# Kernel optimization log

Hardware: AMD Instinct MI355X
Metric: run time of the kernel (lower is better)

Reference implementation:

```python
import jax, jax.numpy as jnp
import numpy as np

V = 50000   # words_num
D = 128     # embedding_dim
B = 2048    # batch
P = 20      # max Huffman path length


def setup_inputs() -> dict:
    key = jax.random.key(0)
    k1, k2, k3, k4, k5 = jax.random.split(key, 5)
    inputs_vector = jax.random.uniform(k1, (B, V), dtype=jnp.float32)
    path_nodes_indices = jax.random.randint(k2, (B, P), 0, V)
    huffman_codes = jax.random.randint(k3, (B, P), 0, 2).astype(jnp.float32)
    mask = jnp.ones((B, P), dtype=jnp.float32)
    # learned params, torch nn.Linear weight layout [out, in], kaiming-uniform-ish scale
    W_emb = jax.random.uniform(k4, (D, V), dtype=jnp.float32, minval=-1.0, maxval=1.0) / np.sqrt(V)
    W_cls = jax.random.uniform(k5, (V, D), dtype=jnp.float32, minval=-1.0, maxval=1.0) / np.sqrt(D)
    return {
        "inputs_vector": inputs_vector,
        "W_emb": W_emb,
        "W_cls": W_cls,
        "path_nodes_indices": path_nodes_indices,
        "huffman_codes": huffman_codes,
        "mask": mask,
    }


def _bce_with_logits(logits, targets):
    # numerically stable, elementwise (reduction='none')
    return jnp.maximum(logits, 0.0) - logits * targets + jnp.log1p(jnp.exp(-jnp.abs(logits)))


def reference(inputs_vector, W_emb, W_cls, path_nodes_indices, huffman_codes, mask):
    x = inputs_vector @ W_emb.T              # [B, D]  embedding Linear (no bias)
    logits_full = x @ W_cls.T                # [B, V]  full-vocab cls matmul (as in source)
    logits = jnp.take_along_axis(logits_full, path_nodes_indices, axis=1)  # [B, P]
    loss = _bce_with_logits(logits, huffman_codes)  # [B, P]
    masked_loss = loss * mask
    per_sample = masked_loss.sum(axis=-1) / mask.sum(axis=-1)  # [B]
    return per_sample.mean()
```

## Files before the change

### kernel.cpp

```cpp
#include <hip/hip_runtime.h>
#include <hip/hip_bf16.h>

#define V 50000
#define D 128
#define B 2048
#define P 20

#define BM 256
#define BK 64
#define NSPLIT 64
#define KC 784
#define NMT (B / BM)

typedef float  f32x4   __attribute__((ext_vector_type(4)));
typedef short  bf16x8  __attribute__((ext_vector_type(8)));
typedef unsigned int uint4v __attribute__((ext_vector_type(4)));

__device__ __forceinline__ unsigned int pk2(float a, float b) {
    return (__float_as_uint(b) & 0xFFFF0000u) | (__float_as_uint(a) >> 16);
}
__device__ __forceinline__ unsigned short f2bf(float f) {
    unsigned int u = __float_as_uint(f);
    return (unsigned short)((u + 0x7FFFu + ((u >> 16) & 1u)) >> 16);
}
__device__ __forceinline__ bf16x8 pack8(f32x4 lo, f32x4 hi) {
    union { uint4v u; bf16x8 h; } r;
    r.u.x = pk2(lo[0], lo[1]); r.u.y = pk2(lo[2], lo[3]);
    r.u.z = pk2(hi[0], hi[1]); r.u.w = pk2(hi[2], hi[3]);
    return r.h;
}

__global__ __launch_bounds__(256)
void w2v_wcast(const float* __restrict__ Wemb, unsigned* __restrict__ Wb) {
    const size_t t = (size_t)blockIdx.x * 256 + threadIdx.x;
    const size_t base = t * 8;
    if (base >= (size_t)D * V) return;
    const f32x4* src = reinterpret_cast<const f32x4*>(Wemb + base);
    f32x4 v0 = src[0], v1 = src[1];
    uint4v u;
    u.x = pk2(v0[0], v0[1]); u.y = pk2(v0[2], v0[3]);
    u.z = pk2(v1[0], v1[1]); u.w = pk2(v1[2], v1[3]);
    *reinterpret_cast<uint4v*>(Wb + base / 2) = u;
}

template<int WBF>
__global__ __launch_bounds__(512, 4)
void w2v_gemm(const float* __restrict__ Ain, const void* __restrict__ Wsrc,
              void* __restrict__ part, int use_atomic) {
    __shared__ uint4v smem4[4096];
    char* smem = (char*)smem4;

    const int i   = blockIdx.x;
    const int xcd = i & 7;
    const int j   = i >> 3;
    const int s   = xcd * 8 + (j >> 3);
    const int mt  = j & 7;
    const int m0  = mt * BM;
    const int k0  = s * KC;
    const int k1  = (k0 + KC < V) ? (k0 + KC) : V;

    const int tid  = threadIdx.x;
    const int lane = tid & 63;
    const int wid  = tid >> 6;
    const int fr   = lane & 15;
    const int kg4  = lane >> 4;

    f32x4 acc[2][8] = {};

    const float* Arow0 = Ain + (size_t)(m0 + wid * 32 + fr) * V;
    const float* Arow1 = Arow0 + (size_t)16 * V;

    for (int ks = k0; ks < k1; ks += BK) {
#pragma unroll
        for (int t2 = 0; t2 < 2; ++t2) {
            const int slot = tid + t2 * 512;
            const int d    = slot >> 3;
            const int c8   = slot & 7;
            const int kg   = ks + c8 * 8;
            uint4v u = {0u, 0u, 0u, 0u};
            if (kg < k1) {
                if (WBF) {
                    u = *reinterpret_cast<const uint4v*>(
                        (const unsigned short*)Wsrc + (size_t)d * V + kg);
                } else {
                    const f32x4* sp = reinterpret_cast<const f32x4*>(
                        (const float*)Wsrc + (size_t)d * V + kg);
                    f32x4 v0 = sp[0], v1 = sp[1];
                    u.x = pk2(v0[0], v0[1]); u.y = pk2(v0[2], v0[3]);
                    u.z = pk2(v1[0], v1[1]); u.w = pk2(v1[2], v1[3]);
                }
            }
            const unsigned dst = (unsigned)(d * 128) +
                (((unsigned)(c8 * 16)) ^ ((unsigned)(d & 7) << 4));
            *reinterpret_cast<uint4v*>(smem + dst) = u;
        }

        const int koff = ks + kg4 * 8;
        f32x4 a00l = {0,0,0,0}, a00h = {0,0,0,0}, a01l = {0,0,0,0}, a01h = {0,0,0,0};
        f32x4 a10l = {0,0,0,0}, a10h = {0,0,0,0}, a11l = {0,0,0,0}, a11h = {0,0,0,0};
        {
            const f32x4* p0 = reinterpret_cast<const f32x4*>(Arow0 + koff);
            const f32x4* p1 = reinterpret_cast<const f32x4*>(Arow1 + koff);
            a00l = p0[0]; a00h = p0[1];
            a01l = p1[0]; a01h = p1[1];
        }
        const bool kh1v = (ks + 32 < k1);
        if (kh1v) {
            const f32x4* p0 = reinterpret_cast<const f32x4*>(Arow0 + koff + 32);
            const f32x4* p1 = reinterpret_cast<const f32x4*>(Arow1 + koff + 32);
            a10l = p0[0]; a10h = p0[1];
            a11l = p1[0]; a11h = p1[1];
        }
        __syncthreads();

        {
            const bf16x8 af0 = pack8(a00l, a00h);
            const bf16x8 af1 = pack8(a01l, a01h);
            const unsigned kb = (unsigned)kg4 << 4;
#pragma unroll
            for (int n = 0; n < 8; ++n) {
                const int r = n * 16 + fr;
                const bf16x8 wf = *reinterpret_cast<const bf16x8*>(
                    smem + r * 128 + (kb ^ ((unsigned)(r & 7) << 4)));
                acc[0][n] = __builtin_amdgcn_mfma_f32_16x16x32_bf16(af0, wf, acc[0][n], 0, 0, 0);
                acc[1][n] = __builtin_amdgcn_mfma_f32_16x16x32_bf16(af1, wf, acc[1][n], 0, 0, 0);
            }
        }
        if (kh1v) {
            const bf16x8 af0 = pack8(a10l, a10h);
            const bf16x8 af1 = pack8(a11l, a11h);
            const unsigned kb = 64u + ((unsigned)kg4 << 4);
#pragma unroll
            for (int n = 0; n < 8; ++n) {
                const int r = n * 16 + fr;
                const bf16x8 wf = *reinterpret_cast<const bf16x8*>(
                    smem + r * 128 + (kb ^ ((unsigned)(r & 7) << 4)));
                acc[0][n] = __builtin_amdgcn_mfma_f32_16x16x32_bf16(af0, wf, acc[0][n], 0, 0, 0);
                acc[1][n] = __builtin_amdgcn_mfma_f32_16x16x32_bf16(af1, wf, acc[1][n], 0, 0, 0);
            }
        }
        __syncthreads();
    }

    if (use_atomic) {
        float* outp = (float*)part;
#pragma unroll
        for (int m = 0; m < 2; ++m) {
            const int r0 = m0 + wid * 32 + m * 16 + kg4 * 4;
#pragma unroll
            for (int n = 0; n < 8; ++n) {
                const int c0 = n * 16 + fr;
#pragma unroll
                for (int jj = 0; jj < 4; ++jj)
                    atomicAdd(&outp[(size_t)(r0 + jj) * D + c0], acc[m][n][jj]);
            }
        }
        return;
    }
    unsigned short* Cs = (unsigned short*)smem;
#pragma unroll
    for (int m = 0; m < 2; ++m) {
        const int r0 = wid * 32 + m * 16 + kg4 * 4;
#pragma unroll
        for (int n = 0; n < 8; ++n) {
            const int c0 = n * 16 + fr;
#pragma unroll
            for (int jj = 0; jj < 4; ++jj)
                Cs[(r0 + jj) * 128 + c0] = f2bf(acc[m][n][jj]);
        }
    }
    __syncthreads();
    char* dstb = (char*)part + ((size_t)s * B + m0) * (D * 2);
#pragma unroll
    for (int it = 0; it < 8; ++it) {
        const int off = (it * 512 + tid) * 16;
        uint4v v = *reinterpret_cast<const uint4v*>(smem + off);
        *reinterpret_cast<uint4v*>(dstb + off) = v;
    }
}

__global__ __launch_bounds__(256)
void w2v_loss(const void* __restrict__ part, int nsplit, int part_bf16,
              const float* __restrict__ Wcls, const int* __restrict__ pathIdx,
              const float* __restrict__ codes, const float* __restrict__ mask,
              float* __restrict__ out) {
    const int lane = threadIdx.x & 63;
    const int wid  = threadIdx.x >> 6;
    const int b    = blockIdx.x * 4 + wid;

    float x0 = 0.f, x1 = 0.f;
    if (part_bf16) {
        const unsigned* pb = (const unsigned*)part;
        for (int s = 0; s < nsplit; ++s) {
            unsigned u = pb[((size_t)s * B + b) * 64 + lane];
            x0 += __uint_as_float(u << 16);
            x1 += __uint_as_float(u & 0xFFFF0000u);
        }
    } else {
        const float* pf = (const float*)part;
        const float2 v = *reinterpret_cast<const float2*>(&pf[(size_t)b * D + lane * 2]);
        x0 = v.x; x1 = v.y;
    }

    float lsum = 0.f, msum = 0.f;
#pragma unroll
    for (int p = 0; p < P; ++p) {
        int node = pathIdx[b * P + p];
        const float2 w = *reinterpret_cast<const float2*>(&Wcls[(size_t)node * D + lane * 2]);
        float d = x0 * w.x + x1 * w.y;
#pragma unroll
        for (int off = 1; off < 64; off <<= 1)
            d += __shfl_xor(d, off, 64);
        float t  = codes[b * P + p];
        float mm = mask[b * P + p];
        float loss = fmaxf(d, 0.f) - d * t + log1pf(__expf(-fabsf(d)));
        lsum += loss * mm;
        msum += mm;
    }
    float per = (msum > 0.f) ? (lsum / msum) : 0.f;

    __shared__ float wsum[4];
    if (lane == 0) wsum[wid] = per;
    __syncthreads();
    if (threadIdx.x == 0) {
        float ssum = wsum[0] + wsum[1] + wsum[2] + wsum[3];
        atomicAdd(out, ssum * (1.0f / (float)B));
    }
}

extern "C" void kernel_launch(void* const* d_in, const int* in_sizes, int n_in,
                              void* d_out, int out_size, void* d_ws, size_t ws_size,
                              hipStream_t stream) {
    const float* inputs = (const float*)d_in[0];
    const float* W_emb  = (const float*)d_in[1];
    const float* W_cls  = (const float*)d_in[2];
    const int*   path   = (const int*)  d_in[3];
    const float* codes  = (const float*)d_in[4];
    const float* mask   = (const float*)d_in[5];
    float* out = (float*)d_out;

    hipMemsetAsync(d_out, 0, sizeof(float), stream);

    const size_t wb_bytes  = (size_t)D * V * 2;
    const size_t part_off  = (wb_bytes + 255) & ~(size_t)255;
    const size_t part_need = part_off + (size_t)NSPLIT * B * D * 2;

    if (ws_size >= part_need) {
        unsigned* Wb  = (unsigned*)d_ws;
        char* partp   = (char*)d_ws + part_off;
        w2v_wcast<<<dim3((D * V / 8 + 255) / 256), dim3(256), 0, stream>>>(W_emb, Wb);
        w2v_gemm<1><<<dim3(NMT * NSPLIT), dim3(512), 0, stream>>>(inputs, Wb, partp, 0);
        w2v_loss<<<dim3(B / 4), dim3(256), 0, stream>>>(partp, NSPLIT, 1,
                                                        W_cls, path, codes, mask, out);
    } else {
        hipMemsetAsync(d_ws, 0, (size_t)B * D * sizeof(float), stream);
        w2v_gemm<0><<<dim3(NMT * NSPLIT), dim3(512), 0, stream>>>(inputs, W_emb, d_ws, 1);
        w2v_loss<<<dim3(B / 4), dim3(256), 0, stream>>>(d_ws, 1, 0,
                                                        W_cls, path, codes, mask, out);
    }
}
```

Baseline: 153.0 us.

## Double-buffer bf16 weight tiles via direct global-to-LDS loads in GEMM main loop

For the bf16-weight path, the weight tile is now loaded straight into LDS with global_load_lds into two alternating buffers, prefetching the next K-slice while MFMAs consume the current one. This removes one barrier per iteration and the register round-trip for staging. The swizzle is moved from the LDS address to the global source column so the direct loads can land contiguously. A separate tail step handles the partial K chunk. It uses twice the LDS, and the caller code that selects the template path and sizes shared memory is not shown.

New measurement: 156.2 us. +2.1%, slower.

```diff
diff --git a/kernel.cpp b/kernel.cpp
--- a/kernel.cpp
+++ b/kernel.cpp
@@ -7,7 +7,6 @@
 #define P 20
 
 #define BM 256
-#define BK 64
 #define NSPLIT 64
 #define KC 784
 #define NMT (B / BM)
@@ -28,6 +27,11 @@
     r.u.x = pk2(lo[0], lo[1]); r.u.y = pk2(lo[2], lo[3]);
     r.u.z = pk2(hi[0], hi[1]); r.u.w = pk2(hi[2], hi[3]);
     return r.h;
+}
+__device__ __forceinline__ void gload_lds16(const void* g, void* l) {
+    __builtin_amdgcn_global_load_lds(
+        (const __attribute__((address_space(1))) unsigned int*)g,
+        (__attribute__((address_space(3))) unsigned int*)l, 16, 0, 0);
 }
 
 __global__ __launch_bounds__(256)
@@ -43,7 +47,7 @@
     *reinterpret_cast<uint4v*>(Wb + base / 2) = u;
 }
 
-template<int WBF>
+template<int FAST>
 __global__ __launch_bounds__(512, 4)
 void w2v_gemm(const float* __restrict__ Ain, const void* __restrict__ Wsrc,
               void* __restrict__ part, int use_atomic) {
@@ -58,6 +62,8 @@
     const int m0  = mt * BM;
     const int k0  = s * KC;
     const int k1  = (k0 + KC < V) ? (k0 + KC) : V;
+    const int nfull = (k1 - k0) >> 6;
+    const int ktail = (k1 - k0) & 63;
 
     const int tid  = threadIdx.x;
     const int lane = tid & 63;
@@ -70,76 +76,126 @@
     const float* Arow0 = Ain + (size_t)(m0 + wid * 32 + fr) * V;
     const float* Arow1 = Arow0 + (size_t)16 * V;
 
-    for (int ks = k0; ks < k1; ks += BK) {
+    const unsigned short* Wb = (const unsigned short*)Wsrc;
+    const float*          Wf = (const float*)Wsrc;
+
+    const int drow = wid * 16 + (lane >> 3);
+    const int c8s  = (lane & 7) ^ (drow & 7);
+    const unsigned short* gW0 = Wb + (size_t)drow * V + 8 * c8s;
+    const unsigned short* gW1 = gW0 + (size_t)8 * V;
+    char* lW = smem + (size_t)(wid * 16) * 128;
+
+    auto stage_guard = [&](int buf, int ks) {
 #pragma unroll
         for (int t2 = 0; t2 < 2; ++t2) {
             const int slot = tid + t2 * 512;
             const int d    = slot >> 3;
-            const int c8   = slot & 7;
+            const int c8l  = slot & 7;
+            const int c8   = c8l ^ (d & 7);
             const int kg   = ks + c8 * 8;
             uint4v u = {0u, 0u, 0u, 0u};
             if (kg < k1) {
-                if (WBF) {
-                    u = *reinterpret_cast<const uint4v*>(
-                        (const unsigned short*)Wsrc + (size_t)d * V + kg);
+                if (FAST) {
+                    u = *reinterpret_cast<const uint4v*>(Wb + (size_t)d * V + kg);
                 } else {
-                    const f32x4* sp = reinterpret_cast<const f32x4*>(
-                        (const float*)Wsrc + (size_t)d * V + kg);
+                    const f32x4* sp = reinterpret_cast<const f32x4*>(Wf + (size_t)d * V + kg);
                     f32x4 v0 = sp[0], v1 = sp[1];
                     u.x = pk2(v0[0], v0[1]); u.y = pk2(v0[2], v0[3]);
                     u.z = pk2(v1[0], v1[1]); u.w = pk2(v1[2], v1[3]);
                 }
             }
-            const unsigned dst = (unsigned)(d * 128) +
-                (((unsigned)(c8 * 16)) ^ ((unsigned)(d & 7) << 4));
-            *reinterpret_cast<uint4v*>(smem + dst) = u;
-        }
-
-        const int koff = ks + kg4 * 8;
-        f32x4 a00l = {0,0,0,0}, a00h = {0,0,0,0}, a01l = {0,0,0,0}, a01h = {0,0,0,0};
-        f32x4 a10l = {0,0,0,0}, a10h = {0,0,0,0}, a11l = {0,0,0,0}, a11h = {0,0,0,0};
-        {
+            *reinterpret_cast<uint4v*>(smem + buf * 16384 + d * 128 + c8l * 16) = u;
+        }
+    };
+
+    int buf = 0;
+    if (FAST) {
+        gload_lds16(gW0 + k0, lW);
+        gload_lds16(gW1 + k0, lW + 1024);
+        __syncthreads();
+        for (int t = 0; t < nfull; ++t) {
+            const int ks   = k0 + t * 64;
+            const int koff = ks + kg4 * 8;
             const f32x4* p0 = reinterpret_cast<const f32x4*>(Arow0 + koff);
             const f32x4* p1 = reinterpret_cast<const f32x4*>(Arow1 + koff);
-            a00l = p0[0]; a00h = p0[1];
-            a01l = p1[0]; a01h = p1[1];
-        }
-        const bool kh1v = (ks + 32 < k1);
-        if (kh1v) {
-            const f32x4* p0 = reinterpret_cast<const f32x4*>(Arow0 + koff + 32);
-            const f32x4* p1 = reinterpret_cast<const f32x4*>(Arow1 + koff + 32);
-            a10l = p0[0]; a10h = p0[1];
-            a11l = p1[0]; a11h = p1[1];
-        }
-        __syncthreads();
-
-        {
-            const bf16x8 af0 = pack8(a00l, a00h);
-            const bf16x8 af1 = pack8(a01l, a01h);
-            const unsigned kb = (unsigned)kg4 << 4;
+            const f32x4 a00l = p0[0], a00h = p0[1];
+            const f32x4 a01l = p1[0], a01h = p1[1];
+            const f32x4 a10l = p0[8], a10h = p0[9];
+            const f32x4 a11l = p1[8], a11h = p1[9];
+            if (t + 1 < nfull) {
+                char* nb = smem + (buf ^ 1) * 16384 + (size_t)(wid * 16) * 128;
+                gload_lds16(gW0 + (ks + 64), nb);
+                gload_lds16(gW1 + (ks + 64), nb + 1024);
+            }
+            const bf16x8 af00 = pack8(a00l, a00h), af01 = pack8(a01l, a01h);
+            const bf16x8 af10 = pack8(a10l, a10h), af11 = pack8(a11l, a11h);
+            char* wb = smem + buf * 16384;
+            const unsigned kb0 = (unsigned)kg4 << 4;
 #pragma unroll
             for (int n = 0; n < 8; ++n) {
                 const int r = n * 16 + fr;
-                const bf16x8 wf = *reinterpret_cast<const bf16x8*>(
-                    smem + r * 128 + (kb ^ ((unsigned)(r & 7) << 4)));
-                acc[0][n] = __builtin_amdgcn_mfma_f32_16x16x32_bf16(af0, wf, acc[0][n], 0, 0, 0);
-                acc[1][n] = __builtin_amdgcn_mfma_f32_16x16x32_bf16(af1, wf, acc[1][n], 0, 0, 0);
-            }
-        }
-        if (kh1v) {
-            const bf16x8 af0 = pack8(a10l, a10h);
-            const bf16x8 af1 = pack8(a11l, a11h);
-            const unsigned kb = 64u + ((unsigned)kg4 << 4);
+                const unsigned sw = (unsigned)(r & 7) << 4;
+                const char* rp = wb + r * 128;
+                const bf16x8 wf0 = *reinterpret_cast<const bf16x8*>(rp + (kb0 ^ sw));
+                const bf16x8 wf1 = *reinterpret_cast<const bf16x8*>(rp + ((kb0 + 64u) ^ sw));
+                acc[0][n] = __builtin_amdgcn_mfma_f32_16x16x32_bf16(af00, wf0, acc[0][n], 0, 0, 0);
+                acc[1][n] = __builtin_amdgcn_mfma_f32_16x16x32_bf16(af01, wf0, acc[1][n], 0, 0, 0);
+                acc[0][n] = __builtin_amdgcn_mfma_f32_16x16x32_bf16(af10, wf1, acc[0][n], 0, 0, 0);
+                acc[1][n] = __builtin_amdgcn_mfma_f32_16x16x32_bf16(af11, wf1, acc[1][n], 0, 0, 0);
+            }
+            __syncthreads();
+            buf ^= 1;
+        }
+        if (ktail) {
+            const int ks = k0 + nfull * 64;
+            stage_guard(buf, ks);
+            __syncthreads();
+            const int koff = ks + kg4 * 8;
+            const f32x4* p0 = reinterpret_cast<const f32x4*>(Arow0 + koff);
+            const f32x4* p1 = reinterpret_cast<const f32x4*>(Arow1 + koff);
+            const bf16x8 af00 = pack8(p0[0], p0[1]);
+            const bf16x8 af01 = pack8(p1[0], p1[1]);
+            char* wb = smem + buf * 16384;
+            const unsigned kb0 = (unsigned)kg4 << 4;
 #pragma unroll
             for (int n = 0; n < 8; ++n) {
                 const int r = n * 16 + fr;
-                const bf16x8 wf = *reinterpret_cast<const bf16x8*>(
-                    smem + r * 128 + (kb ^ ((unsigned)(r & 7) << 4)));
-                acc[0][n] = __builtin_amdgcn_mfma_f32_16x16x32_bf16(af0, wf, acc[0][n], 0, 0, 0);
-                acc[1][n] = __builtin_amdgcn_mfma_f32_16x16x32_bf16(af1, wf, acc[1][n], 0, 0, 0);
-            }
-        }
-        __syncthreads();
+                const unsigned sw = (unsigned)(r & 7) << 4;
+                const bf16x8 wf0 = *reinterpret_cast<const bf16x8*>(wb + r * 128 + (kb0 ^ sw));
+                acc[0][n] = __builtin_amdgcn_mfma_f32_16x16x32_bf16(af00, wf0, acc[0][n], 0, 0, 0);
+                acc[1][n] = __builtin_amdgcn_mfma_f32_16x16x32_bf16(af01, wf0, acc[1][n], 0, 0, 0);
+            }
+            __syncthreads();
+        }
+    } else {
+        for (int ks = k0; ks < k1; ks += 64) {
+            stage_guard(0, ks);
+            __syncthreads();
+            const int koff = ks + kg4 * 8;
+            const f32x4* p0 = reinterpret_cast<const f32x4*>(Arow0 + koff);
+            const f32x4* p1 = reinterpret_cast<const f32x4*>(Arow1 + koff);
+            const bf16x8 af00 = pack8(p0[0], p0[1]);
+            const bf16x8 af01 = pack8(p1[0], p1[1]);
+            const bool kh1v = (ks + 32 < k1);
+            bf16x8 af10 = {}, af11 = {};
+            if (kh1v) { af10 = pack8(p0[8], p0[9]); af11 = pack8(p1[8], p1[9]); }
+            const unsigned kb0 = (unsigned)kg4 << 4;
+#pragma unroll
+            for (int n = 0; n < 8; ++n) {
+                const int r = n * 16 + fr;
+                const unsigned sw = (unsigned)(r & 7) << 4;
+                const char* rp = smem + r * 128;
+                const bf16x8 wf0 = *reinterpret_cast<const bf16x8*>(rp + (kb0 ^ sw));
+                acc[0][n] = __builtin_amdgcn_mfma_f32_16x16x32_bf16(af00, wf0, acc[0][n], 0, 0, 0);
+                acc[1][n] = __builtin_amdgcn_mfma_f32_16x16x32_bf16(af01, wf0, acc[1][n], 0, 0, 0);
+                if (kh1v) {
+                    const bf16x8 wf1 = *reinterpret_cast<const bf16x8*>(rp + ((kb0 + 64u) ^ sw));
+                    acc[0][n] = __builtin_amdgcn_mfma_f32_16x16x32_bf16(af10, wf1, acc[0][n], 0, 0, 0);
+                    acc[1][n] = __builtin_amdgcn_mfma_f32_16x16x32_bf16(af11, wf1, acc[1][n], 0, 0, 0);
+                }
+            }
+            __syncthreads();
+        }
     }
 
     if (use_atomic) {
```

## Double-buffer GEMM with direct global-to-LDS loads and padded bf16 weights

Applied to the files above, without the earlier changes.

Restructures the split-K embedding GEMM so that A (fp32) and the bf16 weight tiles stream straight into LDS via global_load_lds in a double-buffered pipeline. The next K step's loads now overlap the current MFMA work. Tiles shrink to BM=128/BK=32 with 256-thread blocks and 48 K-splits. The weight cast pads V to a multiple of the split size so the fast path needs no bounds checks, with a separate tail path for A. In exchange it uses more LDS (48KB) and converts A to bf16 on every LDS read, and the smaller tiles re-read W more often across M tiles.

Measured after the change: 145.0 us. 5.3% less time.

```diff
diff --git a/kernel.cpp b/kernel.cpp
--- a/kernel.cpp
+++ b/kernel.cpp
@@ -6,14 +6,15 @@
 #define B 2048
 #define P 20
 
-#define BM 256
-#define BK 64
-#define NSPLIT 64
-#define KC 784
+#define BM 128
+#define BK 32
+#define NSPLIT 48
+#define KC 1056
+#define VPAD (NSPLIT * KC)
 #define NMT (B / BM)
 
-typedef float  f32x4   __attribute__((ext_vector_type(4)));
-typedef short  bf16x8  __attribute__((ext_vector_type(8)));
+typedef float  f32x4  __attribute__((ext_vector_type(4)));
+typedef short  bf16x8 __attribute__((ext_vector_type(8)));
 typedef unsigned int uint4v __attribute__((ext_vector_type(4)));
 
 __device__ __forceinline__ unsigned int pk2(float a, float b) {
@@ -29,158 +30,183 @@
     r.u.z = pk2(hi[0], hi[1]); r.u.w = pk2(hi[2], hi[3]);
     return r.h;
 }
+__device__ __forceinline__ void gload_lds16(const void* g, void* l) {
+    __builtin_amdgcn_global_load_lds(
+        (const __attribute__((address_space(1))) unsigned int*)g,
+        (__attribute__((address_space(3))) unsigned int*)l, 16, 0, 0);
+}
 
 __global__ __launch_bounds__(256)
-void w2v_wcast(const float* __restrict__ Wemb, unsigned* __restrict__ Wb) {
+void w2v_wcast(const float* __restrict__ Wemb, unsigned short* __restrict__ Wb) {
     const size_t t = (size_t)blockIdx.x * 256 + threadIdx.x;
+    const size_t n = (size_t)D * VPAD / 8;
+    if (t >= n) return;
     const size_t base = t * 8;
-    if (base >= (size_t)D * V) return;
-    const f32x4* src = reinterpret_cast<const f32x4*>(Wemb + base);
-    f32x4 v0 = src[0], v1 = src[1];
-    uint4v u;
-    u.x = pk2(v0[0], v0[1]); u.y = pk2(v0[2], v0[3]);
-    u.z = pk2(v1[0], v1[1]); u.w = pk2(v1[2], v1[3]);
-    *reinterpret_cast<uint4v*>(Wb + base / 2) = u;
-}
-
-template<int WBF>
-__global__ __launch_bounds__(512, 4)
+    const int d = (int)(base / VPAD);
+    const int k = (int)(base % VPAD);
+    uint4v u = {0u, 0u, 0u, 0u};
+    if (k + 8 <= V) {
+        const f32x4* src = reinterpret_cast<const f32x4*>(Wemb + (size_t)d * V + k);
+        f32x4 v0 = src[0], v1 = src[1];
+        u.x = pk2(v0[0], v0[1]); u.y = pk2(v0[2], v0[3]);
+        u.z = pk2(v1[0], v1[1]); u.w = pk2(v1[2], v1[3]);
+    }
+    *reinterpret_cast<uint4v*>(Wb + (size_t)d * VPAD + k) = u;
+}
+
+template<int FAST>
+__global__ __launch_bounds__(256, 3)
 void w2v_gemm(const float* __restrict__ Ain, const void* __restrict__ Wsrc,
-              void* __restrict__ part, int use_atomic) {
-    __shared__ uint4v smem4[4096];
-    char* smem = (char*)smem4;
+              void* __restrict__ part) {
+    __shared__ char smem[49152];
 
     const int i   = blockIdx.x;
     const int xcd = i & 7;
-    const int j   = i >> 3;
-    const int s   = xcd * 8 + (j >> 3);
-    const int mt  = j & 7;
+    const int q   = i >> 3;
+    const int s   = xcd * 6 + (q >> 4);
+    const int mt  = q & 15;
     const int m0  = mt * BM;
     const int k0  = s * KC;
     const int k1  = (k0 + KC < V) ? (k0 + KC) : V;
+    const int nfull  = (k1 - k0) >> 5;
+    const int ktail  = (k1 - k0) & 31;
+    const int nsteps = nfull + (ktail ? 1 : 0);
 
     const int tid  = threadIdx.x;
     const int lane = tid & 63;
     const int wid  = tid >> 6;
+    const int w32  = wid * 32;
     const int fr   = lane & 15;
     const int kg4  = lane >> 4;
 
     f32x4 acc[2][8] = {};
 
-    const float* Arow0 = Ain + (size_t)(m0 + wid * 32 + fr) * V;
-    const float* Arow1 = Arow0 + (size_t)16 * V;
-
-    for (int ks = k0; ks < k1; ks += BK) {
-#pragma unroll
-        for (int t2 = 0; t2 < 2; ++t2) {
-            const int slot = tid + t2 * 512;
-            const int d    = slot >> 3;
-            const int c8   = slot & 7;
-            const int kg   = ks + c8 * 8;
-            uint4v u = {0u, 0u, 0u, 0u};
-            if (kg < k1) {
-                if (WBF) {
-                    u = *reinterpret_cast<const uint4v*>(
-                        (const unsigned short*)Wsrc + (size_t)d * V + kg);
-                } else {
-                    const f32x4* sp = reinterpret_cast<const f32x4*>(
-                        (const float*)Wsrc + (size_t)d * V + kg);
+    const int arow = w32 + (lane >> 3);
+    const int csrc = (lane & 7) ^ (lane >> 3);
+    const float* aSrc = Ain + (size_t)(m0 + arow) * V + csrc * 4;
+
+    const unsigned short* WbP = (const unsigned short*)Wsrc;
+    const float*          WfP = (const float*)Wsrc;
+    const int wrow = w32 + (lane >> 2);
+    const unsigned short* wSrc = WbP + (size_t)wrow * VPAD + (lane & 3) * 8;
+
+    auto stageA = [&](int buf, int ks) {
+#pragma unroll
+        for (int j = 0; j < 4; ++j)
+            gload_lds16(aSrc + ks + (size_t)j * 8 * V,
+                        smem + buf * 16384 + w32 * 128 + j * 1024);
+    };
+    auto stageW = [&](int buf, int ks) {
+        if (FAST) {
+#pragma unroll
+            for (int j = 0; j < 2; ++j)
+                gload_lds16(wSrc + ks + (size_t)j * 16 * VPAD,
+                            smem + 32768 + buf * 8192 + w32 * 64 + j * 1024);
+        } else {
+#pragma unroll
+            for (int j = 0; j < 2; ++j) {
+                const int slot = tid + j * 256;
+                const int d    = slot >> 2;
+                const int cp   = slot & 3;
+                const int kg   = ks + cp * 8;
+                uint4v u = {0u, 0u, 0u, 0u};
+                if (kg + 8 <= V) {
+                    const f32x4* sp = reinterpret_cast<const f32x4*>(WfP + (size_t)d * V + kg);
                     f32x4 v0 = sp[0], v1 = sp[1];
                     u.x = pk2(v0[0], v0[1]); u.y = pk2(v0[2], v0[3]);
                     u.z = pk2(v1[0], v1[1]); u.w = pk2(v1[2], v1[3]);
                 }
+                *reinterpret_cast<uint4v*>(smem + 32768 + buf * 8192 + d * 64 + cp * 16) = u;
             }
-            const unsigned dst = (unsigned)(d * 128) +
-                (((unsigned)(c8 * 16)) ^ ((unsigned)(d & 7) << 4));
-            *reinterpret_cast<uint4v*>(smem + dst) = u;
-        }
-
-        const int koff = ks + kg4 * 8;
-        f32x4 a00l = {0,0,0,0}, a00h = {0,0,0,0}, a01l = {0,0,0,0}, a01h = {0,0,0,0};
-        f32x4 a10l = {0,0,0,0}, a10h = {0,0,0,0}, a11l = {0,0,0,0}, a11h = {0,0,0,0};
-        {
-            const f32x4* p0 = reinterpret_cast<const f32x4*>(Arow0 + koff);
-            const f32x4* p1 = reinterpret_cast<const f32x4*>(Arow1 + koff);
-            a00l = p0[0]; a00h = p0[1];
-            a01l = p1[0]; a01h = p1[1];
-        }
-        const bool kh1v = (ks + 32 < k1);
-        if (kh1v) {
-            const f32x4* p0 = reinterpret_cast<const f32x4*>(Arow0 + koff + 32);
-            const f32x4* p1 = reinterpret_cast<const f32x4*>(Arow1 + koff + 32);
-            a10l = p0[0]; a10h = p0[1];
-            a11l = p1[0]; a11h = p1[1];
+        }
+    };
+    auto stageAtail = [&](int buf, int ks) {
+#pragma unroll
+        for (int j = 0; j < 4; ++j) {
+            const int slot = tid + j * 256;
+            const int row  = slot >> 3;
+            const int cp   = slot & 7;
+            const int cd   = cp ^ (row & 7);
+            const int kg   = ks + cd * 4;
+            f32x4 v = {0.f, 0.f, 0.f, 0.f};
+            if (kg + 4 <= V)
+                v = *reinterpret_cast<const f32x4*>(Ain + (size_t)(m0 + row) * V + kg);
+            *reinterpret_cast<f32x4*>(smem + buf * 16384 + row * 128 + cp * 16) = v;
+        }
+    };
+
+    int cur = 0;
+    if (nfull > 0) stageA(0, k0); else stageAtail(0, k0);
+    stageW(0, k0);
+    __syncthreads();
+
+    for (int t = 0; t < nsteps; ++t) {
+        const int tn = t + 1;
+        if (tn < nsteps) {
+            const int ksn = k0 + tn * 32;
+            if (tn < nfull) stageA(cur ^ 1, ksn); else stageAtail(cur ^ 1, ksn);
+            stageW(cur ^ 1, ksn);
+        }
+        const char* Ab = smem + cur * 16384;
+        const char* Wl = smem + 32768 + cur * 8192;
+        bf16x8 af[2];
+        const int c0 = (2 * kg4) ^ (fr & 7);
+#pragma unroll
+        for (int m = 0; m < 2; ++m) {
+            const char* rb = Ab + (w32 + m * 16 + fr) * 128;
+            f32x4 lo = *reinterpret_cast<const f32x4*>(rb + c0 * 16);
+            f32x4 hi = *reinterpret_cast<const f32x4*>(rb + (c0 ^ 1) * 16);
+            af[m] = pack8(lo, hi);
+        }
+#pragma unroll
+        for (int n = 0; n < 8; ++n) {
+            const bf16x8 wf = *reinterpret_cast<const bf16x8*>(Wl + (n * 16 + fr) * 64 + kg4 * 16);
+            acc[0][n] = __builtin_amdgcn_mfma_f32_16x16x32_bf16(af[0], wf, acc[0][n], 0, 0, 0);
+            acc[1][n] = __builtin_amdgcn_mfma_f32_16x16x32_bf16(af[1], wf, acc[1][n], 0, 0, 0);
         }
         __syncthreads();
-
-        {
-            const bf16x8 af0 = pack8(a00l, a00h);
-            const bf16x8 af1 = pack8(a01l, a01h);
-            const unsigned kb = (unsigned)kg4 << 4;
+        cur ^= 1;
+    }
+
+    if (!FAST) {
+        float* outp = (float*)part;
+#pragma unroll
+        for (int m = 0; m < 2; ++m) {
+            const int r0 = m0 + w32 + m * 16 + kg4 * 4;
 #pragma unroll
             for (int n = 0; n < 8; ++n) {
-                const int r = n * 16 + fr;
-                const bf16x8 wf = *reinterpret_cast<const bf16x8*>(
-                    smem + r * 128 + (kb ^ ((unsigned)(r & 7) << 4)));
-                acc[0][n] = __builtin_amdgcn_mfma_f32_16x16x32_bf16(af0, wf, acc[0][n], 0, 0, 0);
-                acc[1][n] = __builtin_amdgcn_mfma_f32_16x16x32_bf16(af1, wf, acc[1][n], 0, 0, 0);
+                const int c = n * 16 + fr;
+#pragma unroll
+                for (int jj = 0; jj < 4; ++jj)
+                    atomicAdd(&outp[(size_t)(r0 + jj) * D + c], acc[m][n][jj]);
             }
         }
-        if (kh1v) {
-            const bf16x8 af0 = pack8(a10l, a10h);
-            const bf16x8 af1 = pack8(a11l, a11h);
-            const unsigned kb = 64u + ((unsigned)kg4 << 4);
-#pragma unroll
-            for (int n = 0; n < 8; ++n) {
-                const int r = n * 16 + fr;
-                const bf16x8 wf = *reinterpret_cast<const bf16x8*>(
-                    smem + r * 128 + (kb ^ ((unsigned)(r & 7) << 4)));
-                acc[0][n] = __builtin_amdgcn_mfma_f32_16x16x32_bf16(af0, wf, acc[0][n], 0, 0, 0);
-                acc[1][n] = __builtin_amdgcn_mfma_f32_16x16x32_bf16(af1, wf, acc[1][n], 0, 0, 0);
-            }
-        }
-        __syncthreads();
-    }
-
-    if (use_atomic) {
-        float* outp = (float*)part;
-#pragma unroll
-        for (int m = 0; m < 2; ++m) {
-            const int r0 = m0 + wid * 32 + m * 16 + kg4 * 4;
-#pragma unroll
-            for (int n = 0; n < 8; ++n) {
-                const int c0 = n * 16 + fr;
-#pragma unroll
-                for (int jj = 0; jj < 4; ++jj)
-                    atomicAdd(&outp[(size_t)(r0 + jj) * D + c0], acc[m][n][jj]);
-            }
-        }
         return;
     }
     unsigned short* Cs = (unsigned short*)smem;
 #pragma unroll
     for (int m = 0; m < 2; ++m) {
-        const int r0 = wid * 32 + m * 16 + kg4 * 4;
+        const int r0 = w32 + m * 16 + kg4 * 4;
 #pragma unroll
         for (int n = 0; n < 8; ++n) {
-            const int c0 = n * 16 + fr;
+            const int c = n * 16 + fr;
 #pragma unroll
             for (int jj = 0; jj < 4; ++jj)
-                Cs[(r0 + jj) * 128 + c0] = f2bf(acc[m][n][jj]);
+                Cs[(r0 + jj) * 128 + c] = f2bf(acc[m][n][jj]);
         }
     }
     __syncthreads();
     char* dstb = (char*)part + ((size_t)s * B + m0) * (D * 2);
 #pragma unroll
     for (int it = 0; it < 8; ++it) {
-        const int off = (it * 512 + tid) * 16;
+        const int off = (it * 256 + tid) * 16;
         uint4v v = *reinterpret_cast<const uint4v*>(smem + off);
         *reinterpret_cast<uint4v*>(dstb + off) = v;
     }
 }
 
 __global__ __launch_bounds__(256)
-void w2v_loss(const void* __restrict__ part, int nsplit, int part_bf16,
+void w2v_loss(const void* __restrict__ part, int part_bf16,
               const float* __restrict__ Wcls, const int* __restrict__ pathIdx,
               const float* __restrict__ codes, const float* __restrict__ mask,
               float* __restrict__ out) {
@@ -191,7 +217,8 @@
     float x0 = 0.f, x1 = 0.f;
     if (part_bf16) {
         const unsigned* pb = (const unsigned*)part;
-        for (int s = 0; s < nsplit; ++s) {
+#pragma unroll 8
+        for (int s = 0; s < NSPLIT; ++s) {
             unsigned u = pb[((size_t)s * B + b) * 64 + lane];
             x0 += __uint_as_float(u << 16);
             x1 += __uint_as_float(u & 0xFFFF0000u);
@@ -241,21 +268,19 @@
 
     hipMemsetAsync(d_out, 0, sizeof(float), stream);
 
-    const size_t wb_bytes  = (size_t)D * V * 2;
+    const size_t wb_bytes  = (size_t)D * VPAD * 2;
     const size_t part_off  = (wb_bytes + 255) & ~(size_t)255;
     const size_t part_need = part_off + (size_t)NSPLIT * B * D * 2;
 
     if (ws_size >= part_need) {
-        unsigned* Wb  = (unsigned*)d_ws;
-        char* partp   = (char*)d_ws + part_off;
-        w2v_wcast<<<dim3((D * V / 8 + 255) / 256), dim3(256), 0, stream>>>(W_emb, Wb);
-        w2v_gemm<1><<<dim3(NMT * NSPLIT), dim3(512), 0, stream>>>(inputs, Wb, partp, 0);
-        w2v_loss<<<dim3(B / 4), dim3(256), 0, stream>>>(partp, NSPLIT, 1,
-                                                        W_cls, path, codes, mask, out);
+        unsigned short* Wb = (unsigned short*)d_ws;
+        char* partp = (char*)d_ws + part_off;
+        w2v_wcast<<<dim3((unsigned)((size_t)D * VPAD / 8 / 256)), dim3(256), 0, stream>>>(W_emb, Wb);
+        w2v_gemm<1><<<dim3(NMT * NSPLIT), dim3(256), 0, stream>>>(inputs, Wb, partp);
+        w2v_loss<<<dim3(B / 4), dim3(256), 0, stream>>>(partp, 1, W_cls, path, codes, mask, out);
     } else {
         hipMemsetAsync(d_ws, 0, (size_t)B * D * sizeof(float), stream);
-        w2v_gemm<0><<<dim3(NMT * NSPLIT), dim3(512), 0, stream>>>(inputs, W_emb, d_ws, 1);
-        w2v_loss<<<dim3(B / 4), dim3(256), 0, stream>>>(d_ws, 1, 0,
-                                                        W_cls, path, codes, mask, out);
-    }
-}
+        w2v_gemm<0><<<dim3(NMT * NSPLIT), dim3(256), 0, stream>>>(inputs, W_emb, d_ws);
+        w2v_loss<<<dim3(B / 4), dim3(256), 0, stream>>>(d_ws, 0, W_cls, path, codes, mask, out);
+    }
+}
```
